# Optimization experiments

Hardware: AMD Instinct MI355X
Metric: run time of the kernel (lower is better)

## Reference

```python
import jax, jax.numpy as jnp
import numpy as np

B, S, D_MODEL = 2, 1024, 768
NUM_HEADS = 12
HEAD_DIM = D_MODEL // NUM_HEADS  # 64
W_ONE_SIDED = 32  # attention_window = 64 total (symmetric band of 2w+1 = 65)
OUT_DIM = 768


def setup_inputs() -> dict:
    key = jax.random.key(0)
    ks = jax.random.split(key, 6)
    s = 0.02
    return {
        "layer_embeddings": jax.random.normal(ks[0], (B, S, D_MODEL), jnp.float32),
        "Wq": jax.random.normal(ks[1], (D_MODEL, D_MODEL), jnp.float32) * s,
        "bq": jnp.zeros((D_MODEL,), jnp.float32),
        "Wk": jax.random.normal(ks[2], (D_MODEL, D_MODEL), jnp.float32) * s,
        "bk": jnp.zeros((D_MODEL,), jnp.float32),
        "Wv": jax.random.normal(ks[3], (D_MODEL, D_MODEL), jnp.float32) * s,
        "bv": jnp.zeros((D_MODEL,), jnp.float32),
        "Wfc": jax.random.normal(ks[4], (D_MODEL, OUT_DIM), jnp.float32) * s,
        "bfc": jnp.zeros((OUT_DIM,), jnp.float32),
    }


def reference(layer_embeddings, Wq, bq, Wk, bk, Wv, bv, Wfc, bfc):
    x = layer_embeddings                          # [B, S, D]
    b, s_len, d = x.shape
    q = (x @ Wq + bq).reshape(b, s_len, NUM_HEADS, HEAD_DIM)
    k = (x @ Wk + bk).reshape(b, s_len, NUM_HEADS, HEAD_DIM)
    v = (x @ Wv + bv).reshape(b, s_len, NUM_HEADS, HEAD_DIM)

    w = W_ONE_SIDED
    offs = jnp.arange(-w, w + 1)                  # [band]
    pos = jnp.arange(s_len)[:, None] + offs[None, :]  # [S, band]
    valid = (pos >= 0) & (pos < s_len)
    idx = jnp.clip(pos, 0, s_len - 1)

    # Gather only the banded keys/values (honors the sliding-window sparsity)
    kb = k[:, idx]                                # [B, S, band, H, Dh]
    vb = v[:, idx]                                # [B, S, band, H, Dh]

    scale = 1.0 / np.sqrt(HEAD_DIM).astype(np.float32)
    scores = jnp.einsum('bshd,bswhd->bhsw', q, kb) * scale  # [B, H, S, band]
    scores = jnp.where(valid[None, None, :, :], scores, jnp.float32(-1e9))
    attn = jax.nn.softmax(scores, axis=-1)

    out = jnp.einsum('bhsw,bswhd->bshd', attn, vb).reshape(b, s_len, d)
    pooled = out.mean(axis=1)                     # [B, D]
    return jax.nn.relu(pooled @ Wfc + bfc)        # [B, OUT_DIM]
```

## Files before the change

kernel.cpp:

```cpp
#include <hip/hip_runtime.h>
#include <hip/hip_bf16.h>
#include <stdint.h>

#define S_LEN 1024
#define BATCH 2
#define DM    768
#define NH    12
#define HD    64
#define W1    32
#define WIN   65
#define NQKV  2304
#define M_TOT 2048

typedef unsigned short u16;
typedef __attribute__((ext_vector_type(4))) float f4;
typedef __attribute__((ext_vector_type(4))) unsigned short us4;
typedef __attribute__((ext_vector_type(8))) unsigned short ushort8;
typedef __attribute__((ext_vector_type(8))) __bf16 bf16x8;
typedef __attribute__((ext_vector_type(4))) float f32x4;

__device__ inline u16 f2bf(float x) {
    union { float f; unsigned u; } z;
    z.f = x;
    unsigned r = z.u + 0x7FFF + ((z.u >> 16) & 1);
    return (u16)(r >> 16);
}

__device__ __forceinline__ void g2l16(const u16* g, u16* l) {
    __builtin_amdgcn_global_load_lds(
        (const __attribute__((address_space(1))) unsigned int*)g,
        (__attribute__((address_space(3))) unsigned int*)l, 16, 0, 0);
}

__global__ __launch_bounds__(256) void prep(
    const float* __restrict__ X,
    const float* __restrict__ Wq, const float* __restrict__ Wk,
    const float* __restrict__ Wv,
    u16* __restrict__ Xb, u16* __restrict__ Wt) {
    __shared__ float tile[64][69];
    const int t = threadIdx.x;
    const int bid = blockIdx.x;

    if (bid < 768) {
        const long base = (long)bid * 2048 + t * 8;
        f4 a = *(const f4*)&X[base];
        f4 b = *(const f4*)&X[base + 4];
        float v[8] = {a.x, a.y, a.z, a.w, b.x, b.y, b.z, b.w};
        ushort8 h;
        #pragma unroll
        for (int j = 0; j < 8; ++j) h[j] = f2bf(v[j]);
        *(ushort8*)&Xb[base] = h;
    } else {
        const int tw = bid - 768;
        const int n0 = (tw % 36) * 64;
        const int k0 = (tw / 36) * 64;
        const int sel = n0 / DM;
        const int nl0 = n0 % DM;
        const float* W = (sel == 0) ? Wq : ((sel == 1) ? Wk : Wv);
        const int r = t >> 3;
        const int cg8 = t & 7;

        #pragma unroll
        for (int p = 0; p < 2; ++p) {
            int rr = r + p * 32;
            long gb = (long)(k0 + rr) * DM + nl0 + cg8 * 8;
            *(f4*)&tile[rr][cg8 * 8]     = *(const f4*)&W[gb];
            *(f4*)&tile[rr][cg8 * 8 + 4] = *(const f4*)&W[gb + 4];
        }
        __syncthreads();
        #pragma unroll
        for (int p = 0; p < 2; ++p) {
            int rn = r + p * 32;
            ushort8 h;
            #pragma unroll
            for (int jj = 0; jj < 8; ++jj)
                h[jj] = f2bf(tile[cg8 * 8 + jj][rn]);
            *(ushort8*)&Wt[(long)(n0 + rn) * DM + k0 + cg8 * 8] = h;
        }
    }
}

__global__ __launch_bounds__(256) void qkv_gemm_mfma(
    const u16* __restrict__ Xb, const u16* __restrict__ Wt,
    const float* __restrict__ bq, const float* __restrict__ bk,
    const float* __restrict__ bv,
    u16* __restrict__ Q, u16* __restrict__ K, u16* __restrict__ Vt) {
    __shared__ u16 As[2][128 * 64];
    __shared__ u16 Bs[2][64 * 64];

    const int bid = blockIdx.x;
    const int xcd = bid & 7;
    const int local = bid >> 3;
    const int mt = (xcd & 1) * 8 + (local & 7);
    const int nt = (xcd >> 1) * 9 + (local >> 3);
    const int m0 = mt * 128;
    const int n0 = nt * 64;
    const int t = threadIdx.x;
    const int lane = t & 63;
    const int w = t >> 6;
    const int wm = w * 32;
    const int lrow = lane & 15;
    const int lq = lane >> 4;

    const u16* gA[4];
    const u16* gB[2];
    #pragma unroll
    for (int p = 0; p < 4; ++p) {
        int slot = p * 256 + t;
        int row = slot >> 3;
        int skc = (slot & 7) ^ (row & 7);
        gA[p] = Xb + (long)(m0 + row) * DM + skc * 8;
    }
    #pragma unroll
    for (int p = 0; p < 2; ++p) {
        int slot = p * 256 + t;
        int row = slot >> 3;
        int skc = (slot & 7) ^ (row & 7);
        gB[p] = Wt + (long)(n0 + row) * DM + skc * 8;
    }

#define STAGE(buf)                                                          \
    do {                                                                    \
        _Pragma("unroll")                                                   \
        for (int p = 0; p < 4; ++p)                                         \
            g2l16(gA[p], &As[buf][(p * 256 + w * 64) * 8]);                 \
        _Pragma("unroll")                                                   \
        for (int p = 0; p < 2; ++p)                                         \
            g2l16(gB[p], &Bs[buf][(p * 256 + w * 64) * 8]);                 \
        _Pragma("unroll")                                                   \
        for (int p = 0; p < 4; ++p) gA[p] += 64;                            \
        _Pragma("unroll")                                                   \
        for (int p = 0; p < 2; ++p) gB[p] += 64;                            \
    } while (0)

    const f32x4 fzero = {0.f, 0.f, 0.f, 0.f};
    f32x4 acc[2][4];
    #pragma unroll
    for (int i = 0; i < 2; ++i)
        #pragma unroll
        for (int j = 0; j < 4; ++j) acc[i][j] = fzero;

    STAGE(0);
    __syncthreads();

    #pragma unroll
    for (int ks = 0; ks < 12; ++ks) {
        const int cb = ks & 1;
        if (ks < 11) STAGE(cb ^ 1);
        #pragma unroll
        for (int kh = 0; kh < 2; ++kh) {
            const int c = kh * 4 + lq;
            bf16x8 ah[2], bh[4];
            #pragma unroll
            for (int i = 0; i < 2; ++i) {
                int ar = wm + i * 16 + lrow;
                ah[i] = *(const bf16x8*)&As[cb][(ar * 8 + (c ^ (ar & 7))) * 8];
            }
            #pragma unroll
            for (int j = 0; j < 4; ++j) {
                int br = j * 16 + lrow;
                bh[j] = *(const bf16x8*)&Bs[cb][(br * 8 + (c ^ (br & 7))) * 8];
            }
            #pragma unroll
            for (int i = 0; i < 2; ++i)
                #pragma unroll
                for (int j = 0; j < 4; ++j)
                    acc[i][j] = __builtin_amdgcn_mfma_f32_16x16x32_bf16(
                        ah[i], bh[j], acc[i][j], 0, 0, 0);
        }
        if (ks < 11) __syncthreads();
    }
#undef STAGE

    const int region = n0 / DM;
    const int nc0 = n0 % DM;
    const float* bias = (region == 0) ? bq : ((region == 1) ? bk : bv);

    if (region < 2) {
        u16* Out = (region == 0) ? Q : K;
        #pragma unroll
        for (int j = 0; j < 4; ++j) {
            int col = nc0 + j * 16 + lrow;
            float bval = bias[col];
            #pragma unroll
            for (int i = 0; i < 2; ++i) {
                int row = m0 + wm + i * 16 + lq * 4;
                #pragma unroll
                for (int r = 0; r < 4; ++r)
                    Out[(long)(row + r) * DM + col] = f2bf(acc[i][j][r] + bval);
            }
        }
    } else {
        const int h = nc0 >> 6;
        #pragma unroll
        for (int j = 0; j < 4; ++j) {
            int dloc = j * 16 + lrow;
            float bval = bias[nc0 + dloc];
            #pragma unroll
            for (int i = 0; i < 2; ++i) {
                int row = m0 + wm + i * 16 + lq * 4;
                int b = row >> 10, sl = row & 1023;
                us4 pk;
                #pragma unroll
                for (int r = 0; r < 4; ++r) pk[r] = f2bf(acc[i][j][r] + bval);
                *(us4*)&Vt[(((long)(b * NH + h) * 64 + dloc) << 10) + sl] = pk;
            }
        }
    }
}

__global__ __launch_bounds__(128) void attn_pool_mfma(
    const u16* __restrict__ Q, const u16* __restrict__ K,
    const u16* __restrict__ Vt, float* __restrict__ partial) {
    __shared__ u16 pl[2][16][104];
    __shared__ float pr[2][64];
    const int b = blockIdx.z, h = blockIdx.y;
    const int bx = blockIdx.x;
    const int s0 = bx * 32;
    const int t = threadIdx.x;
    const int k0 = s0 - 32;

    const u16* vtg = Vt + ((size_t)(b * NH + h) * 64) * 1024;
    const int w = t >> 6, lane = t & 63;
    const int cl = lane & 15, q = lane >> 4;

    const f32x4 fzero = {0.f, 0.f, 0.f, 0.f};
    f32x4 accS[6];
    #pragma unroll
    for (int n = 0; n < 6; ++n) accS[n] = fzero;

    const long qrow = (long)(b * S_LEN + s0 + w * 16 + cl);
    bf16x8 aq[2];
    #pragma unroll
    for (int ks = 0; ks < 2; ++ks)
        aq[ks] = *(const bf16x8*)&Q[qrow * DM + h * HD + ks * 32 + q * 8];
    #pragma unroll
    for (int n = 0; n < 6; ++n) {
        int key = k0 + n * 16 + cl;
        int kcl = key < 0 ? 0 : (key > S_LEN - 1 ? S_LEN - 1 : key);
        long ka = (long)(b * S_LEN + kcl) * DM + h * HD;
        #pragma unroll
        for (int ks = 0; ks < 2; ++ks) {
            bf16x8 bk8 = *(const bf16x8*)&K[ka + ks * 32 + q * 8];
            accS[n] = __builtin_amdgcn_mfma_f32_16x16x32_bf16(aq[ks], bk8, accS[n], 0, 0, 0);
        }
    }

    float l4[4] = {0.f, 0.f, 0.f, 0.f};
    #pragma unroll
    for (int n = 0; n < 6; ++n) {
        int key = k0 + n * 16 + cl;
        #pragma unroll
        for (int r = 0; r < 4; ++r) {
            int s = s0 + w * 16 + q * 4 + r;
            bool valid = (key >= s - W1) && (key <= s + W1) && (key >= 0) && (key < S_LEN);
            float p = valid ? __expf(accS[n][r] * 0.125f) : 0.f;
            accS[n][r] = p;
            l4[r] += p;
        }
    }
    #pragma unroll
    for (int m = 1; m <= 8; m <<= 1)
        #pragma unroll
        for (int r = 0; r < 4; ++r) l4[r] += __shfl_xor(l4[r], m, 64);

    #pragma unroll
    for (int n = 0; n < 6; ++n)
        #pragma unroll
        for (int r = 0; r < 4; ++r)
            pl[w][q * 4 + r][n * 16 + cl] = f2bf(accS[n][r]);

    f32x4 accO[4];
    #pragma unroll
    for (int n = 0; n < 4; ++n) accO[n] = fzero;
    bf16x8 ap[3];
    #pragma unroll
    for (int ks = 0; ks < 3; ++ks)
        ap[ks] = *(const bf16x8*)&pl[w][cl][ks * 32 + q * 8];

    const bool edge = (bx == 0) || (bx == 31);
    #pragma unroll
    for (int n = 0; n < 4; ++n) {
        const u16* vrow = &vtg[(size_t)(n * 16 + cl) * 1024];
        #pragma unroll
        for (int ks = 0; ks < 3; ++ks) {
            int kb = k0 + ks * 32 + q * 8;
            bf16x8 bv8;
            if (!edge) {
                bv8 = *(const bf16x8*)&vrow[kb];
            } else {
                union { ushort8 u; bf16x8 bfv; } cvt;
                #pragma unroll
                for (int j = 0; j < 8; ++j) {
                    int kk = kb + j;
                    int kcl = kk < 0 ? 0 : (kk > S_LEN - 1 ? S_LEN - 1 : kk);
                    cvt.u[j] = vrow[kcl];
                }
                bv8 = cvt.bfv;
            }
            accO[n] = __builtin_amdgcn_mfma_f32_16x16x32_bf16(ap[ks], bv8, accO[n], 0, 0, 0);
        }
    }

    float rcp4[4];
    #pragma unroll
    for (int r = 0; r < 4; ++r) rcp4[r] = 1.0f / l4[r];
    #pragma unroll
    for (int n = 0; n < 4; ++n) {
        float pp = 0.f;
        #pragma unroll
        for (int r = 0; r < 4; ++r) pp += accO[n][r] * rcp4[r];
        pp += __shfl_xor(pp, 16, 64);
        pp += __shfl_xor(pp, 32, 64);
        if (q == 0) pr[w][n * 16 + cl] = pp;
    }
    __syncthreads();
    if (t < 64) {
        long pb = (((long)(b * NH + h) * 32) + bx) * 64 + t;
        partial[pb] = pr[0][t] + pr[1][t];
    }
}

__global__ __launch_bounds__(256) void fc_relu_f(
    const float* __restrict__ partial, const float* __restrict__ Wfc,
    const float* __restrict__ bfc, float* __restrict__ out) {
    __shared__ float red[4][64];
    __shared__ float ps[768];
    const int t = threadIdx.x;
    const int nb = blockIdx.x % 12;
    const int bb = blockIdx.x / 12;

    for (int d = t; d < DM; d += 256) {
        const float* pp = partial + ((long)(bb * NH + (d >> 6)) * 32) * 64 + (d & 63);
        float s = 0.f;
        #pragma unroll
        for (int sb = 0; sb < 32; ++sb) s += pp[sb * 64];
        ps[d] = s;
    }
    __syncthreads();

    const int nn = t & 63;
    const int dg = t >> 6;
    const int n = nb * 64 + nn;
    float s = 0.f;
    for (int d = dg * 192; d < dg * 192 + 192; ++d)
        s += ps[d] * Wfc[(long)d * DM + n];
    red[dg][nn] = s;
    __syncthreads();
    if (t < 64) {
        float sum = red[0][t] + red[1][t] + red[2][t] + red[3][t];
        sum = sum * (1.0f / (float)S_LEN) + bfc[nb * 64 + t];
        sum = sum > 0.f ? sum : 0.f;
        out[bb * DM + nb * 64 + t] = sum;
    }
}

extern "C" void kernel_launch(void* const* d_in, const int* in_sizes, int n_in,
                              void* d_out, int out_size, void* d_ws, size_t ws_size,
                              hipStream_t stream) {
    const float* X   = (const float*)d_in[0];
    const float* Wq  = (const float*)d_in[1];
    const float* bq  = (const float*)d_in[2];
    const float* Wk  = (const float*)d_in[3];
    const float* bk  = (const float*)d_in[4];
    const float* Wv  = (const float*)d_in[5];
    const float* bv  = (const float*)d_in[6];
    const float* Wfc = (const float*)d_in[7];
    const float* bfc = (const float*)d_in[8];

    char* ws = (char*)d_ws;
    const size_t SZ_XB = (size_t)M_TOT * DM * 2;
    const size_t SZ_WB = (size_t)NQKV * DM * 2;
    u16* Xb = (u16*)(ws);
    u16* Wt = (u16*)(ws + SZ_XB);
    u16* Qp = (u16*)(ws + SZ_XB + SZ_WB);
    u16* Kp = (u16*)(ws + 2 * SZ_XB + SZ_WB);
    u16* Vt = (u16*)(ws + 3 * SZ_XB + SZ_WB);
    float* partial = (float*)(ws + 4 * SZ_XB + SZ_WB);

    prep<<<1200, 256, 0, stream>>>(X, Wq, Wk, Wv, Xb, Wt);

    qkv_gemm_mfma<<<576, 256, 0, stream>>>(
        Xb, Wt, bq, bk, bv, Qp, Kp, Vt);

    attn_pool_mfma<<<dim3(32, NH, BATCH), 128, 0, stream>>>(
        Qp, Kp, Vt, partial);

    fc_relu_f<<<24, 256, 0, stream>>>(partial, Wfc, bfc, (float*)d_out);
}
```

Before: 130.0 us.

## Retile QKV GEMM to 64x96, stage V band in LDS, split FC wider

The QKV GEMM moves from 128x64 tiles (576 blocks) to 64x96 tiles (768 blocks), with a new XCD-aware block mapping. Each wave now computes a 16x96 strip with one A fragment and six B fragments. The attention kernel first loads the 96-key V^T band into shared memory, with clamping at the sequence edges, and then feeds the MFMAs from LDS instead of strided global reads. The FC kernel doubles its grid to 48 blocks of 32 outputs each, and each block reduces over eight d-groups. These changes aim to raise occupancy and parallelism and to cut uncoalesced global V reads, at the cost of lower A-reuse per wave in the GEMM and one extra LDS sync.

```diff
diff --git a/kernel.cpp b/kernel.cpp
--- a/kernel.cpp
+++ b/kernel.cpp
@@ -85,34 +85,34 @@
     const float* __restrict__ bq, const float* __restrict__ bk,
     const float* __restrict__ bv,
     u16* __restrict__ Q, u16* __restrict__ K, u16* __restrict__ Vt) {
-    __shared__ u16 As[2][128 * 64];
-    __shared__ u16 Bs[2][64 * 64];
+    __shared__ u16 As[2][64 * 64];
+    __shared__ u16 Bs[2][96 * 64];
 
     const int bid = blockIdx.x;
     const int xcd = bid & 7;
     const int local = bid >> 3;
-    const int mt = (xcd & 1) * 8 + (local & 7);
-    const int nt = (xcd >> 1) * 9 + (local >> 3);
-    const int m0 = mt * 128;
-    const int n0 = nt * 64;
+    const int nt = local % 24;
+    const int mt = (xcd << 2) + (local / 24);
+    const int m0 = mt * 64;
+    const int n0 = nt * 96;
     const int t = threadIdx.x;
     const int lane = t & 63;
     const int w = t >> 6;
-    const int wm = w * 32;
+    const int wm = w * 16;
     const int lrow = lane & 15;
     const int lq = lane >> 4;
 
-    const u16* gA[4];
-    const u16* gB[2];
-    #pragma unroll
-    for (int p = 0; p < 4; ++p) {
+    const u16* gA[2];
+    const u16* gB[3];
+    #pragma unroll
+    for (int p = 0; p < 2; ++p) {
         int slot = p * 256 + t;
         int row = slot >> 3;
         int skc = (slot & 7) ^ (row & 7);
         gA[p] = Xb + (long)(m0 + row) * DM + skc * 8;
     }
     #pragma unroll
-    for (int p = 0; p < 2; ++p) {
+    for (int p = 0; p < 3; ++p) {
         int slot = p * 256 + t;
         int row = slot >> 3;
         int skc = (slot & 7) ^ (row & 7);
@@ -122,23 +122,21 @@
 #define STAGE(buf)                                                          \
     do {                                                                    \
         _Pragma("unroll")                                                   \
-        for (int p = 0; p < 4; ++p)                                         \
+        for (int p = 0; p < 2; ++p)                                         \
             g2l16(gA[p], &As[buf][(p * 256 + w * 64) * 8]);                 \
         _Pragma("unroll")                                                   \
-        for (int p = 0; p < 2; ++p)                                         \
+        for (int p = 0; p < 3; ++p)                                         \
             g2l16(gB[p], &Bs[buf][(p * 256 + w * 64) * 8]);                 \
         _Pragma("unroll")                                                   \
-        for (int p = 0; p < 4; ++p) gA[p] += 64;                            \
+        for (int p = 0; p < 2; ++p) gA[p] += 64;                            \
         _Pragma("unroll")                                                   \
-        for (int p = 0; p < 2; ++p) gB[p] += 64;                            \
+        for (int p = 0; p < 3; ++p) gB[p] += 64;                            \
     } while (0)
 
     const f32x4 fzero = {0.f, 0.f, 0.f, 0.f};
-    f32x4 acc[2][4];
-    #pragma unroll
-    for (int i = 0; i < 2; ++i)
-        #pragma unroll
-        for (int j = 0; j < 4; ++j) acc[i][j] = fzero;
+    f32x4 acc[6];
+    #pragma unroll
+    for (int j = 0; j < 6; ++j) acc[j] = fzero;
 
     STAGE(0);
     __syncthreads();
@@ -150,23 +148,18 @@
         #pragma unroll
         for (int kh = 0; kh < 2; ++kh) {
             const int c = kh * 4 + lq;
-            bf16x8 ah[2], bh[4];
-            #pragma unroll
-            for (int i = 0; i < 2; ++i) {
-                int ar = wm + i * 16 + lrow;
-                ah[i] = *(const bf16x8*)&As[cb][(ar * 8 + (c ^ (ar & 7))) * 8];
-            }
-            #pragma unroll
-            for (int j = 0; j < 4; ++j) {
+            const int ar = wm + lrow;
+            bf16x8 ah = *(const bf16x8*)&As[cb][(ar * 8 + (c ^ (ar & 7))) * 8];
+            bf16x8 bh[6];
+            #pragma unroll
+            for (int j = 0; j < 6; ++j) {
                 int br = j * 16 + lrow;
                 bh[j] = *(const bf16x8*)&Bs[cb][(br * 8 + (c ^ (br & 7))) * 8];
             }
             #pragma unroll
-            for (int i = 0; i < 2; ++i)
-                #pragma unroll
-                for (int j = 0; j < 4; ++j)
-                    acc[i][j] = __builtin_amdgcn_mfma_f32_16x16x32_bf16(
-                        ah[i], bh[j], acc[i][j], 0, 0, 0);
+            for (int j = 0; j < 6; ++j)
+                acc[j] = __builtin_amdgcn_mfma_f32_16x16x32_bf16(
+                    ah, bh[j], acc[j], 0, 0, 0);
         }
         if (ks < 11) __syncthreads();
     }
@@ -175,36 +168,29 @@
     const int region = n0 / DM;
     const int nc0 = n0 % DM;
     const float* bias = (region == 0) ? bq : ((region == 1) ? bk : bv);
+    const int row = m0 + wm + lq * 4;
 
     if (region < 2) {
         u16* Out = (region == 0) ? Q : K;
         #pragma unroll
-        for (int j = 0; j < 4; ++j) {
+        for (int j = 0; j < 6; ++j) {
             int col = nc0 + j * 16 + lrow;
             float bval = bias[col];
             #pragma unroll
-            for (int i = 0; i < 2; ++i) {
-                int row = m0 + wm + i * 16 + lq * 4;
-                #pragma unroll
-                for (int r = 0; r < 4; ++r)
-                    Out[(long)(row + r) * DM + col] = f2bf(acc[i][j][r] + bval);
-            }
+            for (int r = 0; r < 4; ++r)
+                Out[(long)(row + r) * DM + col] = f2bf(acc[j][r] + bval);
         }
     } else {
-        const int h = nc0 >> 6;
-        #pragma unroll
-        for (int j = 0; j < 4; ++j) {
-            int dloc = j * 16 + lrow;
-            float bval = bias[nc0 + dloc];
-            #pragma unroll
-            for (int i = 0; i < 2; ++i) {
-                int row = m0 + wm + i * 16 + lq * 4;
-                int b = row >> 10, sl = row & 1023;
-                us4 pk;
-                #pragma unroll
-                for (int r = 0; r < 4; ++r) pk[r] = f2bf(acc[i][j][r] + bval);
-                *(us4*)&Vt[(((long)(b * NH + h) * 64 + dloc) << 10) + sl] = pk;
-            }
+        const int b = row >> 10, sl = row & 1023;
+        #pragma unroll
+        for (int j = 0; j < 6; ++j) {
+            int c = nc0 + j * 16 + lrow;
+            int h = c >> 6, dloc = c & 63;
+            float bval = bias[c];
+            us4 pk;
+            #pragma unroll
+            for (int r = 0; r < 4; ++r) pk[r] = f2bf(acc[j][r] + bval);
+            *(us4*)&Vt[(((long)(b * NH + h) * 64 + dloc) << 10) + sl] = pk;
         }
     }
 }
@@ -212,15 +198,33 @@
 __global__ __launch_bounds__(128) void attn_pool_mfma(
     const u16* __restrict__ Q, const u16* __restrict__ K,
     const u16* __restrict__ Vt, float* __restrict__ partial) {
+    __shared__ u16 vt[64][104];
     __shared__ u16 pl[2][16][104];
     __shared__ float pr[2][64];
     const int b = blockIdx.z, h = blockIdx.y;
-    const int bx = blockIdx.x;
-    const int s0 = bx * 32;
+    const int s0 = blockIdx.x * 32;
     const int t = threadIdx.x;
     const int k0 = s0 - 32;
 
     const u16* vtg = Vt + ((size_t)(b * NH + h) * 64) * 1024;
+    #pragma unroll
+    for (int it = 0; it < 6; ++it) {
+        int slot = it * 128 + t;
+        int d = slot / 12, kc = slot % 12;
+        int kbase = k0 + kc * 8;
+        if (kbase >= 0 && kbase + 7 < S_LEN) {
+            *(ushort8*)&vt[d][kc * 8] = *(const ushort8*)&vtg[d * 1024 + kbase];
+        } else {
+            #pragma unroll
+            for (int j = 0; j < 8; ++j) {
+                int kk = kbase + j;
+                int kcl = kk < 0 ? 0 : (kk > S_LEN - 1 ? S_LEN - 1 : kk);
+                vt[d][kc * 8 + j] = vtg[d * 1024 + kcl];
+            }
+        }
+    }
+    __syncthreads();
+
     const int w = t >> 6, lane = t & 63;
     const int cl = lane & 15, q = lane >> 4;
 
@@ -277,30 +281,13 @@
     #pragma unroll
     for (int ks = 0; ks < 3; ++ks)
         ap[ks] = *(const bf16x8*)&pl[w][cl][ks * 32 + q * 8];
-
-    const bool edge = (bx == 0) || (bx == 31);
-    #pragma unroll
-    for (int n = 0; n < 4; ++n) {
-        const u16* vrow = &vtg[(size_t)(n * 16 + cl) * 1024];
+    #pragma unroll
+    for (int n = 0; n < 4; ++n)
         #pragma unroll
         for (int ks = 0; ks < 3; ++ks) {
-            int kb = k0 + ks * 32 + q * 8;
-            bf16x8 bv8;
-            if (!edge) {
-                bv8 = *(const bf16x8*)&vrow[kb];
-            } else {
-                union { ushort8 u; bf16x8 bfv; } cvt;
-                #pragma unroll
-                for (int j = 0; j < 8; ++j) {
-                    int kk = kb + j;
-                    int kcl = kk < 0 ? 0 : (kk > S_LEN - 1 ? S_LEN - 1 : kk);
-                    cvt.u[j] = vrow[kcl];
-                }
-                bv8 = cvt.bfv;
-            }
+            bf16x8 bv8 = *(const bf16x8*)&vt[n * 16 + cl][ks * 32 + q * 8];
             accO[n] = __builtin_amdgcn_mfma_f32_16x16x32_bf16(ap[ks], bv8, accO[n], 0, 0, 0);
         }
-    }
 
     float rcp4[4];
     #pragma unroll
@@ -316,7 +303,7 @@
     }
     __syncthreads();
     if (t < 64) {
-        long pb = (((long)(b * NH + h) * 32) + bx) * 64 + t;
+        long pb = (((long)(b * NH + h) * 32) + blockIdx.x) * 64 + t;
         partial[pb] = pr[0][t] + pr[1][t];
     }
 }
@@ -324,11 +311,11 @@
 __global__ __launch_bounds__(256) void fc_relu_f(
     const float* __restrict__ partial, const float* __restrict__ Wfc,
     const float* __restrict__ bfc, float* __restrict__ out) {
-    __shared__ float red[4][64];
+    __shared__ float red[8][32];
     __shared__ float ps[768];
     const int t = threadIdx.x;
-    const int nb = blockIdx.x % 12;
-    const int bb = blockIdx.x / 12;
+    const int nb = blockIdx.x % 24;
+    const int bb = blockIdx.x / 24;
 
     for (int d = t; d < DM; d += 256) {
         const float* pp = partial + ((long)(bb * NH + (d >> 6)) * 32) * 64 + (d & 63);
@@ -339,19 +326,20 @@
     }
     __syncthreads();
 
-    const int nn = t & 63;
-    const int dg = t >> 6;
-    const int n = nb * 64 + nn;
+    const int nn = t & 31;
+    const int dg = t >> 5;
+    const int n = nb * 32 + nn;
     float s = 0.f;
-    for (int d = dg * 192; d < dg * 192 + 192; ++d)
+    for (int d = dg * 96; d < dg * 96 + 96; ++d)
         s += ps[d] * Wfc[(long)d * DM + n];
     red[dg][nn] = s;
     __syncthreads();
-    if (t < 64) {
-        float sum = red[0][t] + red[1][t] + red[2][t] + red[3][t];
-        sum = sum * (1.0f / (float)S_LEN) + bfc[nb * 64 + t];
+    if (t < 32) {
+        float sum = red[0][t] + red[1][t] + red[2][t] + red[3][t]
+                  + red[4][t] + red[5][t] + red[6][t] + red[7][t];
+        sum = sum * (1.0f / (float)S_LEN) + bfc[nb * 32 + t];
         sum = sum > 0.f ? sum : 0.f;
-        out[bb * DM + nb * 64 + t] = sum;
+        out[bb * DM + nb * 32 + t] = sum;
     }
 }
 
@@ -380,11 +368,11 @@
 
     prep<<<1200, 256, 0, stream>>>(X, Wq, Wk, Wv, Xb, Wt);
 
-    qkv_gemm_mfma<<<576, 256, 0, stream>>>(
+    qkv_gemm_mfma<<<768, 256, 0, stream>>>(
         Xb, Wt, bq, bk, bv, Qp, Kp, Vt);
 
     attn_pool_mfma<<<dim3(32, NH, BATCH), 128, 0, stream>>>(
         Qp, Kp, Vt, partial);
 
-    fc_relu_f<<<24, 256, 0, stream>>>(partial, Wfc, bfc, (float*)d_out);
-}
+    fc_relu_f<<<48, 256, 0, stream>>>(partial, Wfc, bfc, (float*)d_out);
+}
```

New measurement: 115.6 us. -11.1%, faster.
